# Kernel tuning notes

Measured on AMD Instinct MI355X. Metric: run time of the kernel, lower is better.

The kernel has to match this reference:

```python
import jax, jax.numpy as jnp
import numpy as np
from jax import lax

HEADS = 4
DIM_HEAD = 64


def setup_inputs() -> dict:
    key = jax.random.key(0)
    k1, k2, k3 = jax.random.split(key, 3)
    B, C, H, W = 4, 256, 64, 64
    x = jax.random.normal(k1, (B, C, H, W), dtype=jnp.float32)
    # depthwise 3x3 conv weight, groups=C -> OIHW with O=C, I=1
    w_dw = jax.random.normal(k2, (C, 1, 3, 3), dtype=jnp.float32) * 0.1
    # pointwise 1x1 conv weight C -> 3C (stored as [out, in])
    w_pw = jax.random.normal(k3, (3 * C, C), dtype=jnp.float32) * 0.05
    return {"x": x, "w_dw": w_dw, "w_pw": w_pw}


def reference(x, w_dw, w_pw):
    B, C, H, W = x.shape
    S = H * W
    scale = DIM_HEAD ** -0.5
    # depthwise separable conv QKV projection (no bias)
    dw = lax.conv_general_dilated(
        x, w_dw, window_strides=(1, 1), padding=((1, 1), (1, 1)),
        feature_group_count=C, dimension_numbers=("NCHW", "OIHW", "NCHW"))
    qkv = jnp.einsum("bchw,oc->bohw", dw, w_pw)  # [B, 3C, H, W]
    q, k, v = jnp.split(qkv, 3, axis=1)

    def to_heads(t):
        # b (h d) ih iw -> b h (ih iw) d
        t = t.reshape(B, HEADS, DIM_HEAD, S)
        return jnp.transpose(t, (0, 1, 3, 2))  # [B, h, S, d]

    q, k, v = to_heads(q), to_heads(k), to_heads(v)
    dots = jnp.einsum("bhsd,bhtd->bhst", q, k) * scale  # [B, h, S, S]
    attn = jax.nn.softmax(dots, axis=-1)
    out = jnp.einsum("bhst,bhtd->bhsd", attn, v)  # [B, h, S, d]
    # b h (ih iw) d -> b (h d) ih iw
    out = jnp.transpose(out, (0, 1, 3, 2)).reshape(B, C, H, W)
    return out
```

## Files before the change

kernel.cpp:

```cpp
#include <hip/hip_runtime.h>


typedef __attribute__((ext_vector_type(8))) __bf16 bf16x8;
typedef __attribute__((ext_vector_type(4))) float f32x4;
typedef __attribute__((ext_vector_type(16))) float f32x16;
typedef __attribute__((ext_vector_type(8))) unsigned short ushort8;
typedef __attribute__((ext_vector_type(4))) unsigned int uint4v;

#define OFF_DW 0ull
#define OFF_WB 8388608ull
#define OFF_Q  8781824ull
#define OFF_K  17170432ull
#define OFF_V  25559040ull

__device__ __forceinline__ unsigned short f2bf(float x) {
  unsigned u = __builtin_bit_cast(unsigned, x);
  u += 0x7fffu + ((u >> 16) & 1u);
  return (unsigned short)(u >> 16);
}

__device__ __forceinline__ void gld16(const void* g, void* l) {
  __builtin_amdgcn_global_load_lds((const __attribute__((address_space(1))) void*)g,
                                   (__attribute__((address_space(3))) void*)l, 16, 0, 0);
}

__device__ __forceinline__ unsigned cvtpk(float lo, float hi) {
  unsigned r;
  asm("v_cvt_pk_bf16_f32 %0, %1, %2" : "=v"(r) : "v"(lo), "v"(hi));
  return r;
}

__global__ __launch_bounds__(256) void k_wcvt(const float* __restrict__ wpw,
                                              unsigned short* __restrict__ wbf) {
  int idx = blockIdx.x * 256 + threadIdx.x;
  int o = idx >> 8;
  float v = wpw[idx];
  if (o < 256) v *= 0.18033688011112042f;
  wbf[idx] = f2bf(v);
}

__global__ __launch_bounds__(512) void k_dw(const float* __restrict__ x,
                                            const float* __restrict__ wdw,
                                            unsigned short* __restrict__ dwt) {
  __shared__ float tile[64 * 65];
  const int t = threadIdx.x;
  const int h = blockIdx.x;
  const int c0 = blockIdx.y * 64;
  const int b = blockIdx.z;
  const int w = t & 63;
  const int wq = t >> 6;
#pragma unroll
  for (int i = 0; i < 8; ++i) {
    int cl = wq * 8 + i;
    int c = c0 + cl;
    const float* wd = wdw + c * 9;
    const float* xb = x + ((size_t)(b * 256 + c) << 12);
    float acc = 0.f;
#pragma unroll
    for (int ky = 0; ky < 3; ++ky) {
      int hh = h + ky - 1;
      if ((unsigned)hh < 64u) {
        const float* row = xb + hh * 64;
#pragma unroll
        for (int kx = 0; kx < 3; ++kx) {
          int ww = w + kx - 1;
          if ((unsigned)ww < 64u) acc += row[ww] * wd[ky * 3 + kx];
        }
      }
    }
    tile[w * 65 + cl] = acc;
  }
  __syncthreads();
  int sl = t >> 3, cch = (t & 7) * 8;
  ushort8 p0;
#pragma unroll
  for (int j = 0; j < 8; ++j) p0[j] = f2bf(tile[sl * 65 + cch + j]);
  unsigned short* dst = dwt + ((size_t)(b * 4096 + h * 64 + sl)) * 256 + c0 + cch;
  *(ushort8*)dst = p0;
}

__global__ __launch_bounds__(512) void k_pw(const unsigned short* __restrict__ dwt,
                                            const unsigned short* __restrict__ wbf,
                                            unsigned short* __restrict__ q,
                                            unsigned short* __restrict__ k,
                                            unsigned short* __restrict__ v) {
  __shared__ __align__(16) unsigned char smem[114944];
  const int t = threadIdx.x;
  const int lane = t & 63, wv = t >> 6;
  const int s0 = blockIdx.x * 64;
  const int b = blockIdx.y;
  const int vb = ((lane >> 5) << 9) + (((lane & 31) ^ (lane >> 5)) << 4);
  const char* dsrc = (const char*)dwt + ((size_t)(b * 4096 + s0)) * 512;
#pragma unroll
  for (int i = 0; i < 4; ++i) {
    int I = wv * 4 + i;
    int u = ((2 * i) & 7) << 4;
    gld16(dsrc + (size_t)I * 1024 + (vb ^ u), smem + 65536 + I * 1024);
    gld16((const char*)wbf + (size_t)I * 1024 + (vb ^ u), smem + I * 1024);
  }
  asm volatile("s_waitcnt vmcnt(0)" ::: "memory");
  __syncthreads();

  const int c15 = lane & 15, g = lane >> 4;
  const int wo = wv >> 1, ws = wv & 1;
  const int orow = wo * 16 + c15;

#pragma unroll 1
  for (int yy = 0; yy < 12; ++yy) {
    const unsigned char* wbuf = smem + (yy & 1) * 32768;
    if (yy < 11) {
      unsigned char* wnext = smem + ((yy + 1) & 1) * 32768;
#pragma unroll
      for (int i = 0; i < 4; ++i) {
        int I = wv * 4 + i;
        int u = ((2 * i) & 7) << 4;
        gld16((const char*)wbf + (size_t)(yy + 1) * 32768 + (size_t)I * 1024 + (vb ^ u),
              wnext + I * 1024);
      }
    }

    f32x4 acc[2] = {{0,0,0,0},{0,0,0,0}};
#pragma unroll
    for (int kc = 0; kc < 8; ++kc) {
      bf16x8 a = *(const bf16x8*)(wbuf + orow * 512 + (((kc * 4 + g) ^ (orow & 7)) << 4));
#pragma unroll
      for (int nt = 0; nt < 2; ++nt) {
        int srow = (ws * 2 + nt) * 16 + c15;
        bf16x8 bb = *(const bf16x8*)(smem + 65536 + srow * 512 + (((kc * 4 + g) ^ (srow & 7)) << 4));
        acc[nt] = __builtin_amdgcn_mfma_f32_16x16x32_bf16(a, bb, acc[nt], 0, 0, 0);
      }
    }

    const int type = yy >> 2, head = yy & 3;
    const size_t bh = (size_t)(b * 4 + head);
    if (type == 2) {
#pragma unroll
      for (int nt = 0; nt < 2; ++nt)
#pragma unroll
        for (int r = 0; r < 4; ++r) {
          int d = wo * 16 + g * 4 + r;
          int sg = s0 + (ws * 2 + nt) * 16 + c15;
          v[(bh * 64 + d) * 4096 + sg] = f2bf(acc[nt][r]);
        }
    } else {
      float* ol = (float*)(smem + 98304);
#pragma unroll
      for (int nt = 0; nt < 2; ++nt)
#pragma unroll
        for (int r = 0; r < 4; ++r)
          ol[((ws * 2 + nt) * 16 + c15) * 65 + (wo * 16 + g * 4 + r)] = acc[nt][r];
      __syncthreads();
      unsigned short* dst0 = (type == 0) ? q : k;
      int sl = t >> 3, dch = (t & 7) * 8;
      ushort8 p0;
#pragma unroll
      for (int j = 0; j < 8; ++j) p0[j] = f2bf(ol[sl * 65 + dch + j]);
      unsigned short* dst = dst0 + (bh * 4096 + s0 + sl) * 64 + dch;
      *(ushort8*)dst = p0;
    }

    asm volatile("s_waitcnt vmcnt(0)" ::: "memory");
    __syncthreads();
  }
}

__global__ __launch_bounds__(512) void k_attn(const unsigned short* __restrict__ qg,
                                              const unsigned short* __restrict__ kg,
                                              const unsigned short* __restrict__ vg,
                                              float* __restrict__ out) {
  __shared__ __align__(16) unsigned char smem[98304];
  const int t = threadIdx.x;
  const int lane = t & 63, wv = t >> 6;
  const int l31 = lane & 31, hi = lane >> 5;

  const int blk = blockIdx.x;
  const int xcd = blk & 7, idx = blk >> 3;
  const int bh = xcd * 2 + (idx & 1);
  const int s0 = (idx >> 1) * 256;

  const char* qsrc = (const char*)qg + (size_t)bh * 524288 + (size_t)s0 * 128;
  const char* ksrc = (const char*)kg + (size_t)bh * 524288;
  const char* vsrc = (const char*)vg + (size_t)bh * 524288;
  const int vQK = ((lane >> 3) << 7) + (((lane & 7) ^ (lane >> 3)) << 4);
  const int vV  = ((lane >> 3) << 13) + (((lane & 7) ^ (lane >> 3)) << 4);
  int kpoff[2];
  {
#pragma unroll
    for (int i = 0; i < 2; ++i) {
      int I = (wv & 3) * 2 + i;
      int srb = I * 8 + (lane >> 3);
      if (((srb >> 2) + 1) & 2) srb ^= 12;
      kpoff[i] = srb * 128 + (((lane & 7) ^ (lane >> 3)) << 4);
    }
  }

  auto stage = [&](int tt, int bufid) {
    unsigned char* tb = smem + 32768 + bufid * 16384;
    if (wv < 4) {
#pragma unroll
      for (int i = 0; i < 2; ++i) {
        int I = wv * 2 + i;
        gld16(ksrc + (size_t)tt * 8192 + kpoff[i], tb + I * 1024);
      }
    } else {
#pragma unroll
      for (int i = 0; i < 2; ++i) {
        int I = (wv - 4) * 2 + i;
        gld16(vsrc + (size_t)tt * 128 + (size_t)I * 65536 + vV, tb + 8192 + I * 1024);
      }
    }
  };

#pragma unroll
  for (int i = 0; i < 4; ++i) {
    int I = wv * 4 + i;
    gld16(qsrc + (size_t)I * 1024 + vQK, smem + I * 1024);
  }
  stage(0, 0);
  stage(1, 1);
  asm volatile("s_waitcnt vmcnt(0)" ::: "memory");
  __builtin_amdgcn_s_barrier();
  asm volatile("" ::: "memory");

  bf16x8 qf[4];
  {
    int row = wv * 32 + l31;
#pragma unroll
    for (int ks = 0; ks < 4; ++ks)
      qf[ks] = *(const bf16x8*)(smem + row * 128 + (((ks * 2 + hi) ^ (row & 7)) << 4));
  }

  f32x16 O0, O1, lacc;
#pragma unroll
  for (int r = 0; r < 16; ++r) { O0[r] = 0.f; O1[r] = 0.f; lacc[r] = 0.f; }

  uint4v onesu;
  onesu[0] = onesu[1] = onesu[2] = onesu[3] = 0x3F803F80u;
  const bf16x8 onesb = __builtin_bit_cast(bf16x8, onesu);

  auto tile_body = [&](const unsigned char* kb) {
    const unsigned char* vbuf = kb + 8192;
    f32x16 sc0, sc1;
#pragma unroll
    for (int r = 0; r < 16; ++r) { sc0[r] = 0.f; sc1[r] = 0.f; }
    __builtin_amdgcn_s_setprio(1);
#pragma unroll
    for (int ks = 0; ks < 4; ++ks) {
      int sw = ((ks * 2 + hi) ^ (l31 & 7)) << 4;
      bf16x8 kf0 = *(const bf16x8*)(kb + l31 * 128 + sw);
      sc0 = __builtin_amdgcn_mfma_f32_32x32x16_bf16(kf0, qf[ks], sc0, 0, 0, 0);
      bf16x8 kf1 = *(const bf16x8*)(kb + (32 + l31) * 128 + sw);
      sc1 = __builtin_amdgcn_mfma_f32_32x32x16_bf16(kf1, qf[ks], sc1, 0, 0, 0);
    }
    __builtin_amdgcn_s_setprio(0);

#pragma unroll
    for (int r = 0; r < 16; ++r) {
      sc0[r] = __builtin_amdgcn_exp2f(sc0[r]);
      sc1[r] = __builtin_amdgcn_exp2f(sc1[r]);
    }

    uint4v paw[4];
#pragma unroll
    for (int j = 0; j < 4; ++j) {
      paw[0][j] = cvtpk(sc0[2 * j],     sc0[2 * j + 1]);
      paw[1][j] = cvtpk(sc0[8 + 2 * j], sc0[8 + 2 * j + 1]);
      paw[2][j] = cvtpk(sc1[2 * j],     sc1[2 * j + 1]);
      paw[3][j] = cvtpk(sc1[8 + 2 * j], sc1[8 + 2 * j + 1]);
    }

    __builtin_amdgcn_s_setprio(1);
#pragma unroll
    for (int ks = 0; ks < 4; ++ks) {
      bf16x8 pa = __builtin_bit_cast(bf16x8, paw[ks]);
      lacc = __builtin_amdgcn_mfma_f32_32x32x16_bf16(pa, onesb, lacc, 0, 0, 0);
      int sw = ((ks * 2 + hi) ^ (l31 & 7)) << 4;
      bf16x8 v0 = *(const bf16x8*)(vbuf + l31 * 128 + sw);
      O0 = __builtin_amdgcn_mfma_f32_32x32x16_bf16(pa, v0, O0, 0, 0, 0);
      bf16x8 v1 = *(const bf16x8*)(vbuf + (32 + l31) * 128 + sw);
      O1 = __builtin_amdgcn_mfma_f32_32x32x16_bf16(pa, v1, O1, 0, 0, 0);
    }
    __builtin_amdgcn_s_setprio(0);
  };

#pragma unroll 2
  for (int p = 0; p < 32; ++p) {
    if (p < 31) {
      stage(2 * p + 2, (2 * p + 2) & 3);
      stage(2 * p + 3, (2 * p + 3) & 3);
    }
    tile_body(smem + 32768 + ((2 * p) & 3) * 16384);
    tile_body(smem + 32768 + ((2 * p + 1) & 3) * 16384);
    asm volatile("s_waitcnt vmcnt(0)" ::: "memory");
    __builtin_amdgcn_s_barrier();
    asm volatile("" ::: "memory");
  }

  float rn[16];
#pragma unroll
  for (int r = 0; r < 16; ++r) rn[r] = 1.0f / lacc[r];
  float* ep = (float*)(smem + wv * 4608);
  const size_t outbase = (size_t)bh * 262144 + (size_t)(s0 + wv * 32);
#pragma unroll
  for (int dt = 0; dt < 2; ++dt) {
    const f32x16& O = dt ? O1 : O0;
#pragma unroll
    for (int g4 = 0; g4 < 4; ++g4) {
      f32x4 w;
      w[0] = O[4 * g4 + 0] * rn[4 * g4 + 0];
      w[1] = O[4 * g4 + 1] * rn[4 * g4 + 1];
      w[2] = O[4 * g4 + 2] * rn[4 * g4 + 2];
      w[3] = O[4 * g4 + 3] * rn[4 * g4 + 3];
      *(f32x4*)(ep + l31 * 36 + g4 * 8 + hi * 4) = w;
    }
#pragma unroll
    for (int j = 0; j < 4; ++j) {
      int idx2 = j * 64 + lane;
      int d = idx2 >> 3, s4c = idx2 & 7;
      f32x4 vv = *(const f32x4*)(ep + d * 36 + s4c * 4);
      *(f32x4*)(out + outbase + (size_t)(dt * 32 + d) * 4096 + s4c * 4) = vv;
    }
  }
}

extern "C" void kernel_launch(void* const* d_in, const int* in_sizes, int n_in,
                              void* d_out, int out_size, void* d_ws, size_t ws_size,
                              hipStream_t stream) {
  const float* x = (const float*)d_in[0];
  const float* wdw = (const float*)d_in[1];
  const float* wpw = (const float*)d_in[2];
  float* out = (float*)d_out;
  char* ws = (char*)d_ws;
  unsigned short* dwt = (unsigned short*)(ws + OFF_DW);
  unsigned short* wbf = (unsigned short*)(ws + OFF_WB);
  unsigned short* q = (unsigned short*)(ws + OFF_Q);
  unsigned short* k = (unsigned short*)(ws + OFF_K);
  unsigned short* v = (unsigned short*)(ws + OFF_V);

  k_wcvt<<<dim3(768), dim3(256), 0, stream>>>(wpw, wbf);
  k_dw<<<dim3(64, 4, 4), dim3(512), 0, stream>>>(x, wdw, dwt);
  k_pw<<<dim3(64, 4), dim3(512), 0, stream>>>(dwt, wbf, q, k, v);
  k_attn<<<dim3(256), dim3(512), 0, stream>>>(q, k, v, out);
}
```

Baseline: 124.1 us.

## Split attention KV range across two blocks and combine partials in a separate kernel

Templates the attention kernel on KV length and adds a split mode where each block processes half the keys, writing unnormalized outputs and row sums to workspace. A new combine kernel adds the two partials and divides by the summed denominators. Shared memory shrinks to 64KB so two blocks can co-reside per CU, doubling the grid to raise occupancy. This costs an extra partial-output write/read round trip and a kernel launch. The split path only runs when the workspace is large enough.

After: 134.1 us. +8.1%, slower.

```diff
diff --git a/kernel.cpp b/kernel.cpp
--- a/kernel.cpp
+++ b/kernel.cpp
@@ -12,6 +12,9 @@
 #define OFF_Q  8781824ull
 #define OFF_K  17170432ull
 #define OFF_V  25559040ull
+#define OFF_PO 33947648ull
+#define OFF_PL 67502080ull
+#define WS_NEED 68026368ull
 
 __device__ __forceinline__ unsigned short f2bf(float x) {
   unsigned u = __builtin_bit_cast(unsigned, x);
@@ -164,11 +167,14 @@
   }
 }
 
+template <int NKV, bool SPLIT>
 __global__ __launch_bounds__(512) void k_attn(const unsigned short* __restrict__ qg,
                                               const unsigned short* __restrict__ kg,
                                               const unsigned short* __restrict__ vg,
-                                              float* __restrict__ out) {
-  __shared__ __align__(16) unsigned char smem[98304];
+                                              float* __restrict__ out,
+                                              float* __restrict__ po,
+                                              float* __restrict__ pl) {
+  __shared__ __align__(16) unsigned char smem[65536];
   const int t = threadIdx.x;
   const int lane = t & 63, wv = t >> 6;
   const int l31 = lane & 31, hi = lane >> 5;
@@ -176,7 +182,10 @@
   const int blk = blockIdx.x;
   const int xcd = blk & 7, idx = blk >> 3;
   const int bh = xcd * 2 + (idx & 1);
-  const int s0 = (idx >> 1) * 256;
+  const int rest = idx >> 1;
+  const int s0 = (rest & 15) * 256;
+  const int half = SPLIT ? (rest >> 4) : 0;
+  const int kv0 = half * NKV;
 
   const char* qsrc = (const char*)qg + (size_t)bh * 524288 + (size_t)s0 * 128;
   const char* ksrc = (const char*)kg + (size_t)bh * 524288;
@@ -195,7 +204,7 @@
   }
 
   auto stage = [&](int tt, int bufid) {
-    unsigned char* tb = smem + 32768 + bufid * 16384;
+    unsigned char* tb = smem + bufid * 16384;
     if (wv < 4) {
 #pragma unroll
       for (int i = 0; i < 2; ++i) {
@@ -214,10 +223,10 @@
 #pragma unroll
   for (int i = 0; i < 4; ++i) {
     int I = wv * 4 + i;
-    gld16(qsrc + (size_t)I * 1024 + vQK, smem + I * 1024);
-  }
-  stage(0, 0);
-  stage(1, 1);
+    gld16(qsrc + (size_t)I * 1024 + vQK, smem + 32768 + I * 1024);
+  }
+  stage(kv0 + 0, 0);
+  stage(kv0 + 1, 1);
   asm volatile("s_waitcnt vmcnt(0)" ::: "memory");
   __builtin_amdgcn_s_barrier();
   asm volatile("" ::: "memory");
@@ -227,8 +236,11 @@
     int row = wv * 32 + l31;
 #pragma unroll
     for (int ks = 0; ks < 4; ++ks)
-      qf[ks] = *(const bf16x8*)(smem + row * 128 + (((ks * 2 + hi) ^ (row & 7)) << 4));
-  }
+      qf[ks] = *(const bf16x8*)(smem + 32768 + row * 128 + (((ks * 2 + hi) ^ (row & 7)) << 4));
+  }
+  asm volatile("s_waitcnt lgkmcnt(0)" ::: "memory");
+  __builtin_amdgcn_s_barrier();
+  asm volatile("" ::: "memory");
 
   f32x16 O0, O1, lacc;
 #pragma unroll
@@ -283,44 +295,89 @@
     __builtin_amdgcn_s_setprio(0);
   };
 
+  constexpr int NP = NKV / 2;
 #pragma unroll 2
-  for (int p = 0; p < 32; ++p) {
-    if (p < 31) {
-      stage(2 * p + 2, (2 * p + 2) & 3);
-      stage(2 * p + 3, (2 * p + 3) & 3);
-    }
-    tile_body(smem + 32768 + ((2 * p) & 3) * 16384);
-    tile_body(smem + 32768 + ((2 * p + 1) & 3) * 16384);
+  for (int p = 0; p < NP; ++p) {
+    if (p < NP - 1) {
+      stage(kv0 + 2 * p + 2, (2 * p + 2) & 3);
+      stage(kv0 + 2 * p + 3, (2 * p + 3) & 3);
+    }
+    tile_body(smem + ((2 * p) & 3) * 16384);
+    tile_body(smem + ((2 * p + 1) & 3) * 16384);
     asm volatile("s_waitcnt vmcnt(0)" ::: "memory");
     __builtin_amdgcn_s_barrier();
     asm volatile("" ::: "memory");
   }
 
-  float rn[16];
-#pragma unroll
-  for (int r = 0; r < 16; ++r) rn[r] = 1.0f / lacc[r];
-  float* ep = (float*)(smem + wv * 4608);
-  const size_t outbase = (size_t)bh * 262144 + (size_t)(s0 + wv * 32);
-#pragma unroll
-  for (int dt = 0; dt < 2; ++dt) {
-    const f32x16& O = dt ? O1 : O0;
-#pragma unroll
-    for (int g4 = 0; g4 < 4; ++g4) {
-      f32x4 w;
-      w[0] = O[4 * g4 + 0] * rn[4 * g4 + 0];
-      w[1] = O[4 * g4 + 1] * rn[4 * g4 + 1];
-      w[2] = O[4 * g4 + 2] * rn[4 * g4 + 2];
-      w[3] = O[4 * g4 + 3] * rn[4 * g4 + 3];
-      *(f32x4*)(ep + l31 * 36 + g4 * 8 + hi * 4) = w;
-    }
-#pragma unroll
-    for (int j = 0; j < 4; ++j) {
-      int idx2 = j * 64 + lane;
-      int d = idx2 >> 3, s4c = idx2 & 7;
-      f32x4 vv = *(const f32x4*)(ep + d * 36 + s4c * 4);
-      *(f32x4*)(out + outbase + (size_t)(dt * 32 + d) * 4096 + s4c * 4) = vv;
-    }
-  }
+  float* ep = (float*)(smem + wv * 8192);
+  if (SPLIT) {
+    float* pob = po + ((size_t)(half * 16 + bh)) * 262144 + (size_t)(s0 + wv * 32);
+#pragma unroll
+    for (int dt = 0; dt < 2; ++dt) {
+      const f32x16& O = dt ? O1 : O0;
+#pragma unroll
+      for (int g4 = 0; g4 < 4; ++g4) {
+        f32x4 w;
+        w[0] = O[4 * g4 + 0]; w[1] = O[4 * g4 + 1];
+        w[2] = O[4 * g4 + 2]; w[3] = O[4 * g4 + 3];
+        *(f32x4*)(ep + l31 * 36 + g4 * 8 + hi * 4) = w;
+      }
+#pragma unroll
+      for (int j = 0; j < 4; ++j) {
+        int idx2 = j * 64 + lane;
+        int d = idx2 >> 3, s4c = idx2 & 7;
+        f32x4 vv = *(const f32x4*)(ep + d * 36 + s4c * 4);
+        *(f32x4*)(pob + (size_t)(dt * 32 + d) * 4096 + s4c * 4) = vv;
+      }
+    }
+    if (l31 == 0) {
+      float* plo = pl + (size_t)(half * 16 + bh) * 4096 + s0 + wv * 32 + hi * 4;
+#pragma unroll
+      for (int r = 0; r < 16; ++r) plo[(r & 3) + 8 * (r >> 2)] = lacc[r];
+    }
+  } else {
+    float rn[16];
+#pragma unroll
+    for (int r = 0; r < 16; ++r) rn[r] = 1.0f / lacc[r];
+    const size_t outbase = (size_t)bh * 262144 + (size_t)(s0 + wv * 32);
+#pragma unroll
+    for (int dt = 0; dt < 2; ++dt) {
+      const f32x16& O = dt ? O1 : O0;
+#pragma unroll
+      for (int g4 = 0; g4 < 4; ++g4) {
+        f32x4 w;
+        w[0] = O[4 * g4 + 0] * rn[4 * g4 + 0];
+        w[1] = O[4 * g4 + 1] * rn[4 * g4 + 1];
+        w[2] = O[4 * g4 + 2] * rn[4 * g4 + 2];
+        w[3] = O[4 * g4 + 3] * rn[4 * g4 + 3];
+        *(f32x4*)(ep + l31 * 36 + g4 * 8 + hi * 4) = w;
+      }
+#pragma unroll
+      for (int j = 0; j < 4; ++j) {
+        int idx2 = j * 64 + lane;
+        int d = idx2 >> 3, s4c = idx2 & 7;
+        f32x4 vv = *(const f32x4*)(ep + d * 36 + s4c * 4);
+        *(f32x4*)(out + outbase + (size_t)(dt * 32 + d) * 4096 + s4c * 4) = vv;
+      }
+    }
+  }
+}
+
+__global__ __launch_bounds__(256) void k_comb(const float* __restrict__ po,
+                                              const float* __restrict__ pl,
+                                              float* __restrict__ out) {
+  int i4 = blockIdx.x * 256 + threadIdx.x;
+  size_t e = (size_t)i4 * 4;
+  int s2 = (int)((e & 4095) >> 2);
+  int bh = (int)(e >> 18);
+  f32x4 a = ((const f32x4*)po)[i4];
+  f32x4 b = ((const f32x4*)po)[1048576 + i4];
+  f32x4 la = ((const f32x4*)pl)[bh * 1024 + s2];
+  f32x4 lb = ((const f32x4*)pl)[16384 + bh * 1024 + s2];
+  f32x4 o;
+#pragma unroll
+  for (int j = 0; j < 4; ++j) o[j] = (a[j] + b[j]) / (la[j] + lb[j]);
+  ((f32x4*)out)[i4] = o;
 }
 
 extern "C" void kernel_launch(void* const* d_in, const int* in_sizes, int n_in,
@@ -336,9 +393,16 @@
   unsigned short* q = (unsigned short*)(ws + OFF_Q);
   unsigned short* k = (unsigned short*)(ws + OFF_K);
   unsigned short* v = (unsigned short*)(ws + OFF_V);
+  float* po = (float*)(ws + OFF_PO);
+  float* pl = (float*)(ws + OFF_PL);
 
   k_wcvt<<<dim3(768), dim3(256), 0, stream>>>(wpw, wbf);
   k_dw<<<dim3(64, 4, 4), dim3(512), 0, stream>>>(x, wdw, dwt);
   k_pw<<<dim3(64, 4), dim3(512), 0, stream>>>(dwt, wbf, q, k, v);
-  k_attn<<<dim3(256), dim3(512), 0, stream>>>(q, k, v, out);
-}
+  if (ws_size >= WS_NEED) {
+    k_attn<32, true><<<dim3(512), dim3(512), 0, stream>>>(q, k, v, nullptr, po, pl);
+    k_comb<<<dim3(4096), dim3(256), 0, stream>>>(po, pl, out);
+  } else {
+    k_attn<64, false><<<dim3(256), dim3(512), 0, stream>>>(q, k, v, out, nullptr, nullptr);
+  }
+}
```
